# Kernel tuning notes

Hardware: AMD Instinct MI355X
Metric: run time of the kernel (lower is better)

The kernel has to match this reference:

```python
import jax, jax.numpy as jnp
import numpy as np

N, D, NUM_IDS = 4096, 2048, 256
MARGIN = 0.3


def _pairwise_euclidean(x):
    # torch.cdist(x, x, p=2): safe sqrt of squared distances (zero-grad at 0)
    sq = jnp.sum(x * x, axis=1)                      # [N]
    d2 = sq[:, None] + sq[None, :] - 2.0 * (x @ x.T)  # [N, N]
    d2 = jnp.maximum(d2, 0.0)
    d = jnp.sqrt(jnp.where(d2 > 0.0, d2, 1.0))
    return jnp.where(d2 > 0.0, d, 0.0)


def setup_inputs() -> dict:
    key = jax.random.key(0)
    k1, k2 = jax.random.split(key)
    features = jax.random.normal(k1, (N, D), dtype=jnp.float32)
    labels = jax.random.randint(k2, (N,), 0, NUM_IDS, dtype=jnp.int64)
    return {"features": features, "labels": labels}


def reference(features, labels):
    dist = _pairwise_euclidean(features)                     # [N, N]
    mask_pos = labels[None, :] == labels[:, None]            # [N, N] bool
    # batch-hard mining: hardest positive (max), hardest negative (min)
    dist_ap = jnp.max(jnp.where(mask_pos, dist, 0.0), axis=1)       # [N]
    dist_an = jnp.min(jnp.where(mask_pos, jnp.inf, dist), axis=1)   # [N]
    valid = (dist_ap > 0.0) & jnp.isfinite(dist_an)
    # MarginRankingLoss(dist_an, dist_ap, y=1) = mean(relu(dist_ap - dist_an + margin))
    per_anchor = jnp.maximum(dist_ap - dist_an + MARGIN, 0.0)
    n_valid = jnp.sum(valid)
    loss = jnp.sum(jnp.where(valid, per_anchor, 0.0)) / jnp.maximum(n_valid, 1).astype(per_anchor.dtype)
    return jnp.where(n_valid > 0, loss, 0.0)
```

## Files before the change

### kernel.cpp

```cpp
#include <hip/hip_runtime.h>

#define NN 4096
#define DD 2048
#define MARGIN_F 0.3f
#define NTILES 1056
#define BK 256
#define NIT (DD / BK)
#define QS (127.0f / 6.0f)
#define C2 (2.0f * (6.0f / 127.0f) * (6.0f / 127.0f))

typedef __attribute__((ext_vector_type(4))) int i32x4;

__device__ __forceinline__ unsigned q8(float v) {
    int i = __float2int_rn(v * QS);
    i = min(127, max(-127, i));
    return (unsigned)(i & 255);
}

__global__ __launch_bounds__(256) void prep_kernel(const float* __restrict__ x,
                                                   unsigned char* __restrict__ xq,
                                                   float* __restrict__ sq,
                                                   unsigned int* __restrict__ ap,
                                                   unsigned int* __restrict__ an,
                                                   int* __restrict__ counter) {
    const int wave = threadIdx.x >> 6, lane = threadIdx.x & 63;
    const int row = blockIdx.x * 4 + wave;
    const float* xr = x + (size_t)row * DD;
    unsigned int* orow = (unsigned int*)(xq + (size_t)row * DD);
    float s = 0.0f;
#pragma unroll
    for (int j = 0; j < 8; ++j) {
        float4 v = ((const float4*)xr)[j * 64 + lane];
        s += v.x * v.x + v.y * v.y + v.z * v.z + v.w * v.w;
        orow[j * 64 + lane] = q8(v.x) | (q8(v.y) << 8) | (q8(v.z) << 16) | (q8(v.w) << 24);
    }
    for (int off = 32; off > 0; off >>= 1) s += __shfl_down(s, off, 64);
    if (lane == 0) {
        sq[row] = s;
        ap[row] = 0u;
        an[row] = 0x7F800000u;
    }
    if (threadIdx.x == 0 && blockIdx.x == 0) counter[0] = 0;
}

__global__ __launch_bounds__(256) void gemm_reduce_kernel(
    const unsigned char* __restrict__ xq,
    const float* __restrict__ sq,
    const int* __restrict__ labels,
    unsigned int* __restrict__ ap,
    unsigned int* __restrict__ an,
    int* __restrict__ counter,
    float* __restrict__ out) {
    __shared__ __align__(16) unsigned char As[64 * BK];
    __shared__ __align__(16) unsigned char Bs[128 * BK];

    const int orig = blockIdx.x;
    int g = (orig & 7) * (NTILES / 8) + (orig >> 3);
    int si = 0, row_cnt = 244;
    while (g >= row_cnt) { g -= row_cnt; ++si; row_cnt -= 32; }
    int mi64, nj;
    if (g < 20) {
        int ml = 0;
        while (g >= 4 - (ml >> 1)) { g -= 4 - (ml >> 1); ++ml; }
        mi64 = si * 8 + ml;
        nj = si * 4 + (ml >> 1) + g;
    } else {
        g -= 20;
        const int sj = si + 1 + (g >> 5);
        const int r = g & 31;
        mi64 = si * 8 + (r >> 2);
        nj = sj * 4 + (r & 3);
    }
    const int row0 = mi64 * 64;
    const int col0 = nj * 128;
    const int phase = orig & (NIT - 1);

    const int t = threadIdx.x;
    const int lane = t & 63;
    const int wave = t >> 6;
    const int c = lane & 15;
    const int q = lane >> 4;
    const int wc = wave * 32;

    i32x4 acc[4][2];
#pragma unroll
    for (int mi = 0; mi < 4; ++mi)
#pragma unroll
        for (int ni = 0; ni < 2; ++ni)
            acc[mi][ni] = (i32x4){0, 0, 0, 0};

    const int rowb = t >> 4;
    const int colsw = (t & 15) ^ (rowb & 15);
    const unsigned char* gA[4];
    const unsigned char* gB[8];
#pragma unroll
    for (int s = 0; s < 4; ++s)
        gA[s] = xq + (size_t)(row0 + rowb + 16 * s) * DD + colsw * 16;
#pragma unroll
    for (int s = 0; s < 8; ++s)
        gB[s] = xq + (size_t)(col0 + rowb + 16 * s) * DD + colsw * 16;

    for (int it = 0; it < NIT; ++it) {
        const int k0 = ((it + phase) & (NIT - 1)) * BK;
#pragma unroll
        for (int s = 0; s < 4; ++s)
            __builtin_amdgcn_global_load_lds(
                (const __attribute__((address_space(1))) void*)(gA[s] + k0),
                (__attribute__((address_space(3))) void*)&As[(t + 256 * s) * 16],
                16, 0, 0);
#pragma unroll
        for (int s = 0; s < 8; ++s)
            __builtin_amdgcn_global_load_lds(
                (const __attribute__((address_space(1))) void*)(gB[s] + k0),
                (__attribute__((address_space(3))) void*)&Bs[(t + 256 * s) * 16],
                16, 0, 0);
        __syncthreads();

        const i32x4* Av = (const i32x4*)As;
        const i32x4* Bv = (const i32x4*)Bs;
#pragma unroll
        for (int ks = 0; ks < 4; ++ks) {
            const int kc = q + 4 * ks;
            i32x4 af[4], bfr[2];
#pragma unroll
            for (int mi = 0; mi < 4; ++mi) {
                const int r = mi * 16 + c;
                af[mi] = Av[r * 16 + (kc ^ (r & 15))];
            }
#pragma unroll
            for (int ni = 0; ni < 2; ++ni) {
                const int r = wc + ni * 16 + c;
                bfr[ni] = Bv[r * 16 + (kc ^ (r & 15))];
            }
#pragma unroll
            for (int mi = 0; mi < 4; ++mi)
#pragma unroll
                for (int ni = 0; ni < 2; ++ni)
                    acc[mi][ni] = __builtin_amdgcn_mfma_i32_16x16x64_i8(
                        af[mi], bfr[ni], acc[mi][ni], 0, 0, 0);
        }
        __syncthreads();
    }

    float sq_col[2];
    int lab_col[2];
#pragma unroll
    for (int ni = 0; ni < 2; ++ni) {
        const int gj = col0 + wc + ni * 16 + c;
        sq_col[ni] = sq[gj];
        lab_col[ni] = labels[gj];
    }
    int lab_row[4][4];
    float dist[4][2][4];
#pragma unroll
    for (int mi = 0; mi < 4; ++mi) {
#pragma unroll
        for (int r = 0; r < 4; ++r) {
            const int gi = row0 + mi * 16 + q * 4 + r;
            const float sqi = sq[gi];
            lab_row[mi][r] = labels[gi];
#pragma unroll
            for (int ni = 0; ni < 2; ++ni) {
                float d2 = sqi + sq_col[ni] - C2 * (float)acc[mi][ni][r];
                dist[mi][ni][r] = sqrtf(fmaxf(d2, 0.0f));
            }
        }
    }

#pragma unroll
    for (int mi = 0; mi < 4; ++mi) {
#pragma unroll
        for (int r = 0; r < 4; ++r) {
            const int gi = row0 + mi * 16 + q * 4 + r;
            const int li = lab_row[mi][r];
            float apm = 0.0f;
            float anm = __builtin_inff();
#pragma unroll
            for (int ni = 0; ni < 2; ++ni) {
                const int gj = col0 + wc + ni * 16 + c;
                const float d = dist[mi][ni][r];
                if (li == lab_col[ni]) {
                    if (gi != gj) apm = fmaxf(apm, d);
                } else {
                    anm = fminf(anm, d);
                }
            }
#pragma unroll
            for (int off = 1; off < 16; off <<= 1) {
                apm = fmaxf(apm, __shfl_xor(apm, off, 16));
                anm = fminf(anm, __shfl_xor(anm, off, 16));
            }
            if (c == 0) {
                atomicMax(&ap[gi], __float_as_uint(apm));
                atomicMin(&an[gi], __float_as_uint(anm));
            }
        }
    }

#pragma unroll
    for (int ni = 0; ni < 2; ++ni) {
        const int gj = col0 + wc + ni * 16 + c;
        const int lj = lab_col[ni];
        float apm = 0.0f;
        float anm = __builtin_inff();
#pragma unroll
        for (int mi = 0; mi < 4; ++mi) {
#pragma unroll
            for (int r = 0; r < 4; ++r) {
                const int gi = row0 + mi * 16 + q * 4 + r;
                const float d = dist[mi][ni][r];
                if (lj == lab_row[mi][r]) {
                    if (gi != gj) apm = fmaxf(apm, d);
                } else {
                    anm = fminf(anm, d);
                }
            }
        }
        apm = fmaxf(apm, __shfl_xor(apm, 16, 64));
        anm = fminf(anm, __shfl_xor(anm, 16, 64));
        apm = fmaxf(apm, __shfl_xor(apm, 32, 64));
        anm = fminf(anm, __shfl_xor(anm, 32, 64));
        if (q == 0) {
            atomicMax(&ap[gj], __float_as_uint(apm));
            atomicMin(&an[gj], __float_as_uint(anm));
        }
    }

    __syncthreads();
    int* flag = (int*)As;
    if (t == 0) {
        int old = __hip_atomic_fetch_add(counter, 1, __ATOMIC_ACQ_REL,
                                         __HIP_MEMORY_SCOPE_AGENT);
        flag[0] = (old == NTILES - 1) ? 1 : 0;
    }
    __syncthreads();
    if (flag[0]) {
        float sum = 0.0f;
        int cnt = 0;
        for (int i = t; i < NN; i += 256) {
            const float a = __uint_as_float(__hip_atomic_load(
                &ap[i], __ATOMIC_RELAXED, __HIP_MEMORY_SCOPE_AGENT));
            const float b = __uint_as_float(__hip_atomic_load(
                &an[i], __ATOMIC_RELAXED, __HIP_MEMORY_SCOPE_AGENT));
            if ((a > 0.0f) && (b < __builtin_inff())) {
                sum += fmaxf(a - b + MARGIN_F, 0.0f);
                cnt += 1;
            }
        }
        for (int off = 32; off > 0; off >>= 1) {
            sum += __shfl_down(sum, off, 64);
            cnt += __shfl_down(cnt, off, 64);
        }
        float* ssum = (float*)Bs;
        int* scnt = (int*)Bs + 8;
        if (lane == 0) { ssum[wave] = sum; scnt[wave] = cnt; }
        __syncthreads();
        if (t == 0) {
            float s = 0.0f; int n = 0;
#pragma unroll
            for (int w = 0; w < 4; ++w) { s += ssum[w]; n += scnt[w]; }
            out[0] = (n > 0) ? s / (float)n : 0.0f;
        }
    }
}

extern "C" void kernel_launch(void* const* d_in, const int* in_sizes, int n_in,
                              void* d_out, int out_size, void* d_ws, size_t ws_size,
                              hipStream_t stream) {
    const float* x = (const float*)d_in[0];
    const int* labels = (const int*)d_in[1];
    float* out = (float*)d_out;

    char* ws = (char*)d_ws;
    unsigned char* xq = (unsigned char*)ws;
    float* sq = (float*)(ws + (size_t)NN * DD);
    unsigned int* ap = (unsigned int*)(ws + (size_t)NN * DD + (size_t)NN * 4);
    unsigned int* an = (unsigned int*)(ws + (size_t)NN * DD + (size_t)NN * 8);
    int* counter = (int*)(ws + (size_t)NN * DD + (size_t)NN * 12);

    prep_kernel<<<NN / 4, 256, 0, stream>>>(x, xq, sq, ap, an, counter);
    gemm_reduce_kernel<<<NTILES, 256, 0, stream>>>(xq, sq, labels, ap, an, counter, out);
}
```

Baseline: 137.2 us.

## Fuse prep and GEMM-reduce into one cooperative persistent kernel with grid syncs

Replaces the two launches (quantize/norm prep, then int8 GEMM with label-masked min/max reduction) with a single cooperative kernel. It does the prep in a grid-stride loop, runs a grid sync, then processes tiles persistently, and after a second grid sync block 0 computes the final loss. This removes one kernel launch and the atomic-counter last-block finalization. In exchange the grid is capped at the number of resident blocks, so tiles run in multiple waves, and the two grid-wide barriers add their own cost. The old two-kernel path is kept as a fallback if the cooperative launch is unavailable.

```diff
diff --git a/kernel.cpp b/kernel.cpp
--- a/kernel.cpp
+++ b/kernel.cpp
@@ -1,4 +1,7 @@
 #include <hip/hip_runtime.h>
+#include <hip/hip_cooperative_groups.h>
+
+namespace cg = cooperative_groups;
 
 #define NN 4096
 #define DD 2048
@@ -16,6 +19,244 @@
     i = min(127, max(-127, i));
     return (unsigned)(i & 255);
 }
+
+
+__global__ __launch_bounds__(256) void fused_kernel(
+    const float* __restrict__ x,
+    const int* __restrict__ labels,
+    unsigned char* __restrict__ xq,
+    float* __restrict__ sq,
+    unsigned int* __restrict__ ap,
+    unsigned int* __restrict__ an,
+    float* __restrict__ out) {
+    __shared__ __align__(16) unsigned char As[64 * BK];
+    __shared__ __align__(16) unsigned char Bs[128 * BK];
+
+    const int t = threadIdx.x;
+    const int lane = t & 63;
+    const int wave = t >> 6;
+    const int G = gridDim.x;
+
+    for (int row = blockIdx.x * 4 + wave; row < NN; row += G * 4) {
+        const float* xr = x + (size_t)row * DD;
+        unsigned int* orow = (unsigned int*)(xq + (size_t)row * DD);
+        float s = 0.0f;
+#pragma unroll
+        for (int j = 0; j < 8; ++j) {
+            float4 v = ((const float4*)xr)[j * 64 + lane];
+            s += v.x * v.x + v.y * v.y + v.z * v.z + v.w * v.w;
+            orow[j * 64 + lane] =
+                q8(v.x) | (q8(v.y) << 8) | (q8(v.z) << 16) | (q8(v.w) << 24);
+        }
+        for (int off = 32; off > 0; off >>= 1) s += __shfl_down(s, off, 64);
+        if (lane == 0) {
+            sq[row] = s;
+            ap[row] = 0u;
+            an[row] = 0x7F800000u;
+        }
+    }
+    cg::this_grid().sync();
+
+    const int c = lane & 15;
+    const int q = lane >> 4;
+    const int wc = wave * 32;
+    const int rowb = t >> 4;
+    const int colsw = (t & 15) ^ (rowb & 15);
+    const int phase = blockIdx.x & (NIT - 1);
+
+    for (int tid = blockIdx.x; tid < NTILES; tid += G) {
+        int g = (tid & 7) * (NTILES / 8) + (tid >> 3);
+        int si = 0, row_cnt = 244;
+        while (g >= row_cnt) { g -= row_cnt; ++si; row_cnt -= 32; }
+        int mi64, nj;
+        if (g < 20) {
+            int ml = 0;
+            while (g >= 4 - (ml >> 1)) { g -= 4 - (ml >> 1); ++ml; }
+            mi64 = si * 8 + ml;
+            nj = si * 4 + (ml >> 1) + g;
+        } else {
+            g -= 20;
+            const int sj = si + 1 + (g >> 5);
+            const int r = g & 31;
+            mi64 = si * 8 + (r >> 2);
+            nj = sj * 4 + (r & 3);
+        }
+        const int row0 = mi64 * 64;
+        const int col0 = nj * 128;
+
+        i32x4 acc[4][2];
+#pragma unroll
+        for (int mi = 0; mi < 4; ++mi)
+#pragma unroll
+            for (int ni = 0; ni < 2; ++ni)
+                acc[mi][ni] = (i32x4){0, 0, 0, 0};
+
+        const unsigned char* gA[4];
+        const unsigned char* gB[8];
+#pragma unroll
+        for (int s = 0; s < 4; ++s)
+            gA[s] = xq + (size_t)(row0 + rowb + 16 * s) * DD + colsw * 16;
+#pragma unroll
+        for (int s = 0; s < 8; ++s)
+            gB[s] = xq + (size_t)(col0 + rowb + 16 * s) * DD + colsw * 16;
+
+        for (int it = 0; it < NIT; ++it) {
+            const int k0 = ((it + phase) & (NIT - 1)) * BK;
+#pragma unroll
+            for (int s = 0; s < 4; ++s)
+                __builtin_amdgcn_global_load_lds(
+                    (const __attribute__((address_space(1))) void*)(gA[s] + k0),
+                    (__attribute__((address_space(3))) void*)&As[(t + 256 * s) * 16],
+                    16, 0, 0);
+#pragma unroll
+            for (int s = 0; s < 8; ++s)
+                __builtin_amdgcn_global_load_lds(
+                    (const __attribute__((address_space(1))) void*)(gB[s] + k0),
+                    (__attribute__((address_space(3))) void*)&Bs[(t + 256 * s) * 16],
+                    16, 0, 0);
+            __syncthreads();
+
+            const i32x4* Av = (const i32x4*)As;
+            const i32x4* Bv = (const i32x4*)Bs;
+#pragma unroll
+            for (int ks = 0; ks < 4; ++ks) {
+                const int kc = q + 4 * ks;
+                i32x4 af[4], bfr[2];
+#pragma unroll
+                for (int mi = 0; mi < 4; ++mi) {
+                    const int r = mi * 16 + c;
+                    af[mi] = Av[r * 16 + (kc ^ (r & 15))];
+                }
+#pragma unroll
+                for (int ni = 0; ni < 2; ++ni) {
+                    const int r = wc + ni * 16 + c;
+                    bfr[ni] = Bv[r * 16 + (kc ^ (r & 15))];
+                }
+#pragma unroll
+                for (int mi = 0; mi < 4; ++mi)
+#pragma unroll
+                    for (int ni = 0; ni < 2; ++ni)
+                        acc[mi][ni] = __builtin_amdgcn_mfma_i32_16x16x64_i8(
+                            af[mi], bfr[ni], acc[mi][ni], 0, 0, 0);
+            }
+            __syncthreads();
+        }
+
+        float sq_col[2];
+        int lab_col[2];
+#pragma unroll
+        for (int ni = 0; ni < 2; ++ni) {
+            const int gj = col0 + wc + ni * 16 + c;
+            sq_col[ni] = sq[gj];
+            lab_col[ni] = labels[gj];
+        }
+        int lab_row[4][4];
+        float dist[4][2][4];
+#pragma unroll
+        for (int mi = 0; mi < 4; ++mi) {
+#pragma unroll
+            for (int r = 0; r < 4; ++r) {
+                const int gi = row0 + mi * 16 + q * 4 + r;
+                const float sqi = sq[gi];
+                lab_row[mi][r] = labels[gi];
+#pragma unroll
+                for (int ni = 0; ni < 2; ++ni) {
+                    float d2 = sqi + sq_col[ni] - C2 * (float)acc[mi][ni][r];
+                    dist[mi][ni][r] = sqrtf(fmaxf(d2, 0.0f));
+                }
+            }
+        }
+#pragma unroll
+        for (int mi = 0; mi < 4; ++mi) {
+#pragma unroll
+            for (int r = 0; r < 4; ++r) {
+                const int gi = row0 + mi * 16 + q * 4 + r;
+                const int li = lab_row[mi][r];
+                float apm = 0.0f;
+                float anm = __builtin_inff();
+#pragma unroll
+                for (int ni = 0; ni < 2; ++ni) {
+                    const int gj = col0 + wc + ni * 16 + c;
+                    const float d = dist[mi][ni][r];
+                    if (li == lab_col[ni]) {
+                        if (gi != gj) apm = fmaxf(apm, d);
+                    } else {
+                        anm = fminf(anm, d);
+                    }
+                }
+#pragma unroll
+                for (int off = 1; off < 16; off <<= 1) {
+                    apm = fmaxf(apm, __shfl_xor(apm, off, 16));
+                    anm = fminf(anm, __shfl_xor(anm, off, 16));
+                }
+                if (c == 0) {
+                    atomicMax(&ap[gi], __float_as_uint(apm));
+                    atomicMin(&an[gi], __float_as_uint(anm));
+                }
+            }
+        }
+#pragma unroll
+        for (int ni = 0; ni < 2; ++ni) {
+            const int gj = col0 + wc + ni * 16 + c;
+            const int lj = lab_col[ni];
+            float apm = 0.0f;
+            float anm = __builtin_inff();
+#pragma unroll
+            for (int mi = 0; mi < 4; ++mi) {
+#pragma unroll
+                for (int r = 0; r < 4; ++r) {
+                    const int gi = row0 + mi * 16 + q * 4 + r;
+                    const float d = dist[mi][ni][r];
+                    if (lj == lab_row[mi][r]) {
+                        if (gi != gj) apm = fmaxf(apm, d);
+                    } else {
+                        anm = fminf(anm, d);
+                    }
+                }
+            }
+            apm = fmaxf(apm, __shfl_xor(apm, 16, 64));
+            anm = fminf(anm, __shfl_xor(anm, 16, 64));
+            apm = fmaxf(apm, __shfl_xor(apm, 32, 64));
+            anm = fminf(anm, __shfl_xor(anm, 32, 64));
+            if (q == 0) {
+                atomicMax(&ap[gj], __float_as_uint(apm));
+                atomicMin(&an[gj], __float_as_uint(anm));
+            }
+        }
+    }
+
+    cg::this_grid().sync();
+
+    if (blockIdx.x == 0) {
+        float sum = 0.0f;
+        int cnt = 0;
+        for (int i = t; i < NN; i += 256) {
+            const float a = __uint_as_float(__hip_atomic_load(
+                &ap[i], __ATOMIC_RELAXED, __HIP_MEMORY_SCOPE_AGENT));
+            const float b = __uint_as_float(__hip_atomic_load(
+                &an[i], __ATOMIC_RELAXED, __HIP_MEMORY_SCOPE_AGENT));
+            if ((a > 0.0f) && (b < __builtin_inff())) {
+                sum += fmaxf(a - b + MARGIN_F, 0.0f);
+                cnt += 1;
+            }
+        }
+        for (int off = 32; off > 0; off >>= 1) {
+            sum += __shfl_down(sum, off, 64);
+            cnt += __shfl_down(cnt, off, 64);
+        }
+        float* ssum = (float*)Bs;
+        int* scnt = (int*)Bs + 8;
+        if (lane == 0) { ssum[wave] = sum; scnt[wave] = cnt; }
+        __syncthreads();
+        if (t == 0) {
+            float s = 0.0f; int n = 0;
+#pragma unroll
+            for (int w = 0; w < 4; ++w) { s += ssum[w]; n += scnt[w]; }
+            out[0] = (n > 0) ? s / (float)n : 0.0f;
+        }
+    }
+}
+
 
 __global__ __launch_bounds__(256) void prep_kernel(const float* __restrict__ x,
                                                    unsigned char* __restrict__ xq,
@@ -166,7 +407,6 @@
             }
         }
     }
-
 #pragma unroll
     for (int mi = 0; mi < 4; ++mi) {
 #pragma unroll
@@ -196,7 +436,6 @@
             }
         }
     }
-
 #pragma unroll
     for (int ni = 0; ni < 2; ++ni) {
         const int gj = col0 + wc + ni * 16 + c;
@@ -278,6 +517,39 @@
     unsigned int* an = (unsigned int*)(ws + (size_t)NN * DD + (size_t)NN * 8);
     int* counter = (int*)(ws + (size_t)NN * DD + (size_t)NN * 12);
 
-    prep_kernel<<<NN / 4, 256, 0, stream>>>(x, xq, sq, ap, an, counter);
-    gemm_reduce_kernel<<<NTILES, 256, 0, stream>>>(xq, sq, labels, ap, an, counter, out);
+    static int nblk = -2;
+    if (nblk == -2) {
+        int maxb = 0, ncu = 0;
+        hipError_t e1 = hipOccupancyMaxActiveBlocksPerMultiprocessor(
+            &maxb, fused_kernel, 256, 0);
+        hipError_t e2 = hipDeviceGetAttribute(
+            &ncu, hipDeviceAttributeMultiprocessorCount, 0);
+        if (e1 == hipSuccess && e2 == hipSuccess && maxb > 0 && ncu > 0) {
+            long g = (long)maxb * ncu;
+            if (g > NTILES) g = NTILES;
+            g -= g % 8;
+            nblk = (g >= 8) ? (int)g : -1;
+        } else {
+            nblk = -1;
+        }
+    }
+
+    bool launched = false;
+    if (nblk > 0) {
+        void* args[] = {(void*)&x, (void*)&labels, (void*)&xq, (void*)&sq,
+                        (void*)&ap, (void*)&an, (void*)&out};
+        hipError_t e = hipLaunchCooperativeKernel(
+            reinterpret_cast<void*>(fused_kernel), dim3(nblk), dim3(256),
+            args, 0, stream);
+        if (e == hipSuccess) {
+            launched = true;
+        } else {
+            nblk = -1;
+        }
+    }
+    if (!launched) {
+        prep_kernel<<<NN / 4, 256, 0, stream>>>(x, xq, sq, ap, an, counter);
+        gemm_reduce_kernel<<<NTILES, 256, 0, stream>>>(xq, sq, labels, ap, an,
+                                                       counter, out);
+    }
 }
```

Measured after the change: 217.2 us. 1.58x slower.
